# Optimization experiments

Measured on AMD Instinct MI355X. Metric: run time of the kernel, lower is better.

The kernel has to match this reference:

```python
import jax, jax.numpy as jnp
import numpy as np

N = 50000; E = 1600000; F_IN = 32; HEADS = 8; D = 16; HID = HEADS * D
ED = 16; G = 512; MH = 512; MO = 512; SLOPE = 0.2


def setup_inputs() -> dict:
    key = jax.random.key(0)
    ks = jax.random.split(key, 40)
    inp = {}
    inp["x"] = jax.random.normal(ks[0], (N, F_IN), jnp.float32)
    inp["edge_index"] = jax.random.randint(ks[1], (2, E), 0, N)
    inp["edge_attr"] = jax.random.normal(ks[2], (E, ED), jnp.float32)
    inp["batch"] = jnp.sort(jax.random.randint(ks[3], (N,), 0, G))

    def lin(k, fi, fo):
        return jax.random.normal(k, (fi, fo), jnp.float32) / np.sqrt(fi).astype(np.float32)

    i = 4
    dims = [(F_IN, HID), (HID, HID), (HID, HID)]  # GATv2 layers 0..2
    for l, (fi, fo) in enumerate(dims):
        inp[f"Wl{l}"] = lin(ks[i], fi, fo); i += 1
        inp[f"bl{l}"] = jnp.zeros((fo,), jnp.float32)
        inp[f"Wr{l}"] = lin(ks[i], fi, fo); i += 1
        inp[f"br{l}"] = jnp.zeros((fo,), jnp.float32)
        inp[f"We{l}"] = lin(ks[i], ED, fo); i += 1
        inp[f"att{l}"] = jax.random.normal(ks[i], (HEADS, D), jnp.float32) / np.sqrt(D).astype(np.float32); i += 1
        inp[f"b{l}"] = jnp.zeros((fo,), jnp.float32)
    inp["mW1"] = lin(ks[i], HID, MH); i += 1
    inp["mb1"] = jnp.zeros((MH,), jnp.float32)
    inp["ln_g"] = jnp.ones((MH,), jnp.float32)
    inp["ln_b"] = jnp.zeros((MH,), jnp.float32)
    inp["mW2"] = lin(ks[i], MH, MO); i += 1
    inp["mb2"] = jnp.zeros((MO,), jnp.float32)
    return inp


def _gatv2(h, src, dst, ea, Wl, bl, Wr, br, We, att, b):
    # One GATv2Conv layer (eval mode, add_self_loops already applied).
    n = h.shape[0]
    xl = (h @ Wl + bl).reshape(n, HEADS, D)   # source transform
    xr = (h @ Wr + br).reshape(n, HEADS, D)   # target transform
    ee = (ea @ We).reshape(-1, HEADS, D)      # edge transform (no bias in PyG)
    m = xl[src] + xr[dst] + ee                # [E', H, D]
    m = jnp.where(m > 0, m, SLOPE * m)        # LeakyReLU(0.2)
    s = jnp.einsum('ehd,hd->eh', m, att)      # attention logits
    mx = jax.ops.segment_max(s, dst, num_segments=n)
    ex = jnp.exp(s - mx[dst])
    den = jax.ops.segment_sum(ex, dst, num_segments=n)
    alpha = ex / den[dst]                     # softmax over incoming edges
    out = jax.ops.segment_sum(alpha[:, :, None] * xl[src], dst, num_segments=n)
    return out.reshape(n, HEADS * D) + b


def _forward(x, edge_index, edge_attr, batch,
             Wl0, bl0, Wr0, br0, We0, att0, b0,
             Wl1, bl1, Wr1, br1, We1, att1, b1,
             Wl2, bl2, Wr2, br2, We2, att2, b2,
             mW1, mb1, ln_g, ln_b, mW2, mb2):
    src, dst = edge_index[0], edge_index[1]
    # add_self_loops with fill_value='mean': self-loop edge_attr = mean of incoming edge_attr
    cnt = jax.ops.segment_sum(jnp.ones((E,), jnp.float32), dst, num_segments=N)
    loop_attr = jax.ops.segment_sum(edge_attr, dst, num_segments=N) / jnp.clip(cnt, 1.0)[:, None]
    nodes = jnp.arange(N)
    src_f = jnp.concatenate([src, nodes])
    dst_f = jnp.concatenate([dst, nodes])
    ea = jnp.concatenate([edge_attr, loop_attr], axis=0)

    h = jax.nn.relu(_gatv2(x, src_f, dst_f, ea, Wl0, bl0, Wr0, br0, We0, att0, b0))
    h = jax.nn.relu(_gatv2(h, src_f, dst_f, ea, Wl1, bl1, Wr1, br1, We1, att1, b1))
    h = _gatv2(h, src_f, dst_f, ea, Wl2, bl2, Wr2, br2, We2, att2, b2)

    g = jax.ops.segment_sum(h, batch, num_segments=G)  # sum pooling per graph
    z = jax.nn.relu(g @ mW1 + mb1)
    mu = jnp.mean(z, axis=-1, keepdims=True)
    var = jnp.var(z, axis=-1, keepdims=True)
    z = (z - mu) / jnp.sqrt(var + 1e-5) * ln_g + ln_b
    return z @ mW2 + mb2


def reference(x, edge_index, edge_attr, batch,
              Wl0, bl0, Wr0, br0, We0, att0, b0,
              Wl1, bl1, Wr1, br1, We1, att1, b1,
              Wl2, bl2, Wr2, br2, We2, att2, b2,
              mW1, mb1, ln_g, ln_b, mW2, mb2):
    return _forward(x, edge_index, edge_attr, batch,
                    Wl0, bl0, Wr0, br0, We0, att0, b0,
                    Wl1, bl1, Wr1, br1, We1, att1, b1,
                    Wl2, bl2, Wr2, br2, We2, att2, b2,
                    mW1, mb1, ln_g, ln_b, mW2, mb2)
```

## Files before the change

kernel.cpp:

```cpp
#include <hip/hip_runtime.h>
#include <hip/hip_fp16.h>
#include <math.h>

#define NN 50000
#define EE 1600000
#define FIN 32
#define HID_ 128
#define ED_ 16
#define GG 512
#define MH_ 512
#define MO_ 512

typedef float v2f __attribute__((ext_vector_type(2)));

#if __has_builtin(__builtin_amdgcn_exp2f)
#define EXP2(x) __builtin_amdgcn_exp2f(x)
#else
#define EXP2(x) exp2f(x)
#endif

template <int CTRL>
__device__ __forceinline__ float dpp_add(float x) {
  int m = __builtin_amdgcn_update_dpp(0, __float_as_int(x), CTRL, 0xF, 0xF, true);
  return x + __int_as_float(m);
}

__device__ __forceinline__ float bfly8(float p) {
  p = dpp_add<0xB1>(p);
  p = dpp_add<0x4E>(p);
  p = dpp_add<0x141>(p);
  return p;
}

__device__ __forceinline__ v2f h2f(__half2 h) {
  float2 f = __half22float2(h);
  return (v2f){f.x, f.y};
}


__global__ void hist_kernel(const int4* __restrict__ dst4, int* __restrict__ cnt) {
  int e = blockIdx.x * 256 + threadIdx.x;
  if (e >= EE / 4) return;
  int4 d = dst4[e];
  atomicAdd(&cnt[d.x], 1);
  atomicAdd(&cnt[d.y], 1);
  atomicAdd(&cnt[d.z], 1);
  atomicAdd(&cnt[d.w], 1);
}

__global__ __launch_bounds__(256) void scan1_kernel(const int* __restrict__ in, int n,
                                                    int* __restrict__ out,
                                                    int* __restrict__ bsums) {
  int chunk = blockIdx.x;
  int base = chunk * 1024;
  int t = threadIdx.x;
  int idx = base + t * 4;
  int v0 = (idx + 0 < n) ? in[idx + 0] : 0;
  int v1 = (idx + 1 < n) ? in[idx + 1] : 0;
  int v2 = (idx + 2 < n) ? in[idx + 2] : 0;
  int v3 = (idx + 3 < n) ? in[idx + 3] : 0;
  int ts = v0 + v1 + v2 + v3;
  int lane = t & 63, w = t >> 6;
  int s = ts;
#pragma unroll
  for (int off = 1; off < 64; off <<= 1) {
    int o = __shfl_up(s, off);
    if (lane >= off) s += o;
  }
  __shared__ int wsum[4];
  if (lane == 63) wsum[w] = s;
  __syncthreads();
  int woff = 0;
  for (int i = 0; i < w; i++) woff += wsum[i];
  int excl = woff + s - ts;
  int run = excl;
  run += v0; if (idx + 0 < n) out[idx + 0] = run;
  run += v1; if (idx + 1 < n) out[idx + 1] = run;
  run += v2; if (idx + 2 < n) out[idx + 2] = run;
  run += v3; if (idx + 3 < n) out[idx + 3] = run;
  if (t == 255) bsums[chunk] = woff + s;
}

__global__ void scan_add_kernel(int* __restrict__ rowptr, const int* __restrict__ bscan, int n) {
  int i = blockIdx.x * 256 + threadIdx.x;
  if (i == 0) rowptr[0] = 0;
  if (i < n) {
    int chunk = i >> 10;
    if (chunk > 0) rowptr[1 + i] += bscan[chunk - 1];
  }
}

__global__ void scatter_kernel(const int4* __restrict__ src4, const int4* __restrict__ dst4,
                               const int* __restrict__ rowptr, int* __restrict__ fill,
                               int2* __restrict__ csr) {
  int e = blockIdx.x * 256 + threadIdx.x;
  if (e >= EE / 4) return;
  int4 s = src4[e];
  int4 d = dst4[e];
  int eb = e * 4;
  int p0 = rowptr[d.x] + atomicAdd(&fill[d.x], 1);
  csr[p0] = make_int2(s.x, eb + 0);
  int p1 = rowptr[d.y] + atomicAdd(&fill[d.y], 1);
  csr[p1] = make_int2(s.y, eb + 1);
  int p2 = rowptr[d.z] + atomicAdd(&fill[d.z], 1);
  csr[p2] = make_int2(s.z, eb + 2);
  int p3 = rowptr[d.w] + atomicAdd(&fill[d.w], 1);
  csr[p3] = make_int2(s.w, eb + 3);
}


template <int F>
__global__ __launch_bounds__(256) void node_transform(const float* __restrict__ h,
                                                      const float* __restrict__ Wlm,
                                                      const float* __restrict__ blm,
                                                      const float* __restrict__ Wrm,
                                                      const float* __restrict__ brm,
                                                      __half2* __restrict__ xl,
                                                      __half2* __restrict__ xr, int nnodes) {
  __shared__ float hs[F * 34];
  int v0 = blockIdx.x * 32;
  int t = threadIdx.x;
  for (int idx = t; idx < 32 * F; idx += 256) {
    int i = idx / F, k = idx - i * F;
    hs[k * 34 + i] = (v0 + i < nnodes) ? h[(size_t)(v0 + i) * F + k] : 0.f;
  }
  __syncthreads();
  bool isL = t < 128;
  int q = t & 63;
  int nh = (t >> 6) & 1;
  const float* Wm = isL ? Wlm : Wrm;
  v2f acc[16];
#pragma unroll
  for (int i = 0; i < 16; i++) acc[i] = (v2f){0.f, 0.f};
  for (int k = 0; k < F; k++) {
    v2f w = *(const v2f*)(Wm + k * 128 + 2 * q);
    const v2f* hk2 = (const v2f*)(hs + k * 34 + nh * 16);
#pragma unroll
    for (int r = 0; r < 8; r++) {
      v2f hv = hk2[r];
      acc[2 * r + 0] = __builtin_elementwise_fma((v2f){hv.x, hv.x}, w, acc[2 * r + 0]);
      acc[2 * r + 1] = __builtin_elementwise_fma((v2f){hv.y, hv.y}, w, acc[2 * r + 1]);
    }
  }
  const float* bm = isL ? blm : brm;
  v2f b = *(const v2f*)(bm + 2 * q);
  __half2* dstp = isL ? xl : xr;
  int base = v0 + nh * 16;
#pragma unroll
  for (int i = 0; i < 16; i++) {
    if (base + i < nnodes) {
      v2f o = acc[i] + b;
      dstp[(size_t)(base + i) * 64 + q] = __floats2half2_rn(o.x, o.y);
    }
  }
}


template <int LAYER0>
__global__ __launch_bounds__(256) void gat_aggregate(
    const __half2* __restrict__ xl, const __half2* __restrict__ xr,
    const int* __restrict__ rowptr, const int2* __restrict__ csr,
    const float* __restrict__ ea, float* __restrict__ la,
    const float* __restrict__ We, const float* __restrict__ att,
    const float* __restrict__ bias, float* __restrict__ hout, int relu) {
  int wid = threadIdx.x >> 6, lane = threadIdx.x & 63;
  int v = __builtin_amdgcn_readfirstlane(blockIdx.x * 4 + wid);
  if (v >= NN) return;
  int c = 2 * lane;
  v2f wec[16];
#pragma unroll
  for (int k = 0; k < 16; k++) wec[k] = *(const v2f*)(We + k * 128 + c);
  const float L2E = 1.44269504088896340736f;
  v2f av = *(const v2f*)(att + c) * L2E;
  v2f xrv = h2f(xr[(size_t)v * 64 + lane]);

  auto score = [&](int u, const float* eaP, v2f& xu) -> float {
    xu = h2f(xl[(size_t)u * 64 + lane]);
    v2f m = xrv + xu;
#pragma unroll
    for (int k = 0; k < 16; k++) {
      float e = eaP[k];
      m = __builtin_elementwise_fma((v2f){e, e}, wec[k], m);
    }
    m = __builtin_elementwise_max(m, 0.2f * m);
    v2f qq = av * m;
    return bfly8(qq.x + qq.y);
  };

  int d16 = lane & 15;
  v2f acc = (v2f){0.f, 0.f};
  float den = 0.f;
  float la_f = 0.f;
  if (!LAYER0) {
    v2f xu;
    float p = score(v, la + (size_t)v * 16, xu);
    float w = EXP2(p);
    den = w;
    acc = (v2f){w, w} * xu;
  }
  int start = __builtin_amdgcn_readfirstlane(rowptr[v]);
  int end = __builtin_amdgcn_readfirstlane(rowptr[v + 1]);
  int j = start;
  for (; j + 4 <= end; j += 4) {
    int2 e0 = csr[j], e1 = csr[j + 1], e2 = csr[j + 2], e3 = csr[j + 3];
    int u0 = __builtin_amdgcn_readfirstlane(e0.x);
    int u1 = __builtin_amdgcn_readfirstlane(e1.x);
    int u2 = __builtin_amdgcn_readfirstlane(e2.x);
    int u3 = __builtin_amdgcn_readfirstlane(e3.x);
    const float* p0 = ea + (size_t)__builtin_amdgcn_readfirstlane(e0.y) * 16;
    const float* p1 = ea + (size_t)__builtin_amdgcn_readfirstlane(e1.y) * 16;
    const float* p2 = ea + (size_t)__builtin_amdgcn_readfirstlane(e2.y) * 16;
    const float* p3 = ea + (size_t)__builtin_amdgcn_readfirstlane(e3.y) * 16;
    if (LAYER0) la_f += (p0[d16] + p1[d16]) + (p2[d16] + p3[d16]);
    v2f x0, x1, x2, x3;
    float s0 = score(u0, p0, x0);
    float s1 = score(u1, p1, x1);
    float s2 = score(u2, p2, x2);
    float s3 = score(u3, p3, x3);
    float w0 = EXP2(s0), w1 = EXP2(s1), w2 = EXP2(s2), w3 = EXP2(s3);
    den += (w0 + w1) + (w2 + w3);
    acc = __builtin_elementwise_fma((v2f){w0, w0}, x0,
          __builtin_elementwise_fma((v2f){w1, w1}, x1,
          __builtin_elementwise_fma((v2f){w2, w2}, x2,
          __builtin_elementwise_fma((v2f){w3, w3}, x3, acc))));
  }
  for (; j < end; ++j) {
    int2 e0 = csr[j];
    int u = __builtin_amdgcn_readfirstlane(e0.x);
    const float* p0 = ea + (size_t)__builtin_amdgcn_readfirstlane(e0.y) * 16;
    if (LAYER0) la_f += p0[d16];
    v2f xu;
    float p = score(u, p0, xu);
    float w = EXP2(p);
    den += w;
    acc = __builtin_elementwise_fma((v2f){w, w}, xu, acc);
  }
  if (LAYER0) {
    int deg = end - start;
    float invdeg = (deg > 0) ? 1.f / (float)deg : 0.f;
    la_f *= invdeg;
    if (lane < 16) la[(size_t)v * 16 + d16] = la_f;
    v2f xu = h2f(xl[(size_t)v * 64 + lane]);
    v2f m = xrv + xu;
#pragma unroll
    for (int k = 0; k < 16; k++) {
      float e = __int_as_float(__builtin_amdgcn_readlane(__float_as_int(la_f), k));
      m = __builtin_elementwise_fma((v2f){e, e}, wec[k], m);
    }
    m = __builtin_elementwise_max(m, 0.2f * m);
    v2f qq = av * m;
    float p = bfly8(qq.x + qq.y);
    float w = EXP2(p);
    den += w;
    acc = __builtin_elementwise_fma((v2f){w, w}, xu, acc);
  }
  float invd = 1.f / den;
  v2f bv = *(const v2f*)(bias + c);
  v2f o = __builtin_elementwise_fma(acc, (v2f){invd, invd}, bv);
  if (relu) o = __builtin_elementwise_max(o, (v2f){0.f, 0.f});
  *(v2f*)(hout + (size_t)v * 128 + c) = o;
}


__global__ void gptr_kernel(const int* __restrict__ batch, int* __restrict__ gptr) {
  int g = blockIdx.x * 256 + threadIdx.x;
  if (g > GG) return;
  int lo = 0, hi = NN;
  while (lo < hi) {
    int mid = (lo + hi) >> 1;
    if (batch[mid] < g) lo = mid + 1; else hi = mid;
  }
  gptr[g] = lo;
}

__global__ void pool_kernel(const float* __restrict__ h, const int* __restrict__ gptr,
                            float* __restrict__ gp) {
  int gi = blockIdx.x;
  int c = threadIdx.x;
  int s = gptr[gi], e = gptr[gi + 1];
  float acc = 0.f;
  for (int v = s; v < e; v++) acc += h[(size_t)v * 128 + c];
  gp[gi * 128 + c] = acc;
}

__global__ __launch_bounds__(256) void mlp1_kernel(const float* __restrict__ gp,
                                                   const float* __restrict__ mW1,
                                                   const float* __restrict__ mb1,
                                                   const float* __restrict__ lng,
                                                   const float* __restrict__ lnb,
                                                   float* __restrict__ z) {
  int row = blockIdx.x;
  int t = threadIdx.x;
  __shared__ float gs[128];
  if (t < 128) gs[t] = gp[row * 128 + t];
  __syncthreads();
  int c0 = t, c1 = t + 256;
  float z0 = 0.f, z1 = 0.f;
  for (int k = 0; k < 128; k++) {
    float gk = gs[k];
    z0 = fmaf(gk, mW1[k * 512 + c0], z0);
    z1 = fmaf(gk, mW1[k * 512 + c1], z1);
  }
  z0 += mb1[c0]; z1 += mb1[c1];
  z0 = fmaxf(z0, 0.f); z1 = fmaxf(z1, 0.f);
  float s = z0 + z1, q = z0 * z0 + z1 * z1;
#pragma unroll
  for (int off = 32; off > 0; off >>= 1) {
    s += __shfl_xor(s, off);
    q += __shfl_xor(q, off);
  }
  __shared__ float red[8];
  int lane = t & 63, w = t >> 6;
  if (lane == 0) { red[w] = s; red[4 + w] = q; }
  __syncthreads();
  float S = red[0] + red[1] + red[2] + red[3];
  float Q = red[4] + red[5] + red[6] + red[7];
  float mu = S / 512.f;
  float var = Q / 512.f - mu * mu;
  float inv = 1.f / sqrtf(var + 1e-5f);
  z[row * 512 + c0] = (z0 - mu) * inv * lng[c0] + lnb[c0];
  z[row * 512 + c1] = (z1 - mu) * inv * lng[c1] + lnb[c1];
}

__global__ __launch_bounds__(256) void mlp2_kernel(const float* __restrict__ z,
                                                   const float* __restrict__ mW2,
                                                   const float* __restrict__ mb2,
                                                   float* __restrict__ out) {
  int row = blockIdx.x;
  int t = threadIdx.x;
  __shared__ float zs[512];
  for (int i = t; i < 512; i += 256) zs[i] = z[row * 512 + i];
  __syncthreads();
  int c0 = t, c1 = t + 256;
  float o0 = 0.f, o1 = 0.f;
  for (int k = 0; k < 512; k++) {
    float zk = zs[k];
    o0 = fmaf(zk, mW2[k * 512 + c0], o0);
    o1 = fmaf(zk, mW2[k * 512 + c1], o1);
  }
  out[row * 512 + c0] = o0 + mb2[c0];
  out[row * 512 + c1] = o1 + mb2[c1];
}


extern "C" void kernel_launch(void* const* d_in, const int* in_sizes, int n_in,
                              void* d_out, int out_size, void* d_ws, size_t ws_size,
                              hipStream_t stream) {
  const float* x = (const float*)d_in[0];
  const int* ei = (const int*)d_in[1];
  const int* srcE = ei;
  const int* dstE = ei + EE;
  const float* ea = (const float*)d_in[2];
  const int* batch = (const int*)d_in[3];
  const float* Wl[3] = {(const float*)d_in[4], (const float*)d_in[11], (const float*)d_in[18]};
  const float* bl[3] = {(const float*)d_in[5], (const float*)d_in[12], (const float*)d_in[19]};
  const float* Wr[3] = {(const float*)d_in[6], (const float*)d_in[13], (const float*)d_in[20]};
  const float* br[3] = {(const float*)d_in[7], (const float*)d_in[14], (const float*)d_in[21]};
  const float* Wek[3] = {(const float*)d_in[8], (const float*)d_in[15], (const float*)d_in[22]};
  const float* attk[3] = {(const float*)d_in[9], (const float*)d_in[16], (const float*)d_in[23]};
  const float* bk[3] = {(const float*)d_in[10], (const float*)d_in[17], (const float*)d_in[24]};
  const float* mW1 = (const float*)d_in[25];
  const float* mb1 = (const float*)d_in[26];
  const float* lng = (const float*)d_in[27];
  const float* lnb = (const float*)d_in[28];
  const float* mW2 = (const float*)d_in[29];
  const float* mb2 = (const float*)d_in[30];
  float* outp = (float*)d_out;

  char* W = (char*)d_ws;
  size_t off = 0;
  auto take = [&](size_t b) -> void* {
    void* p = W + off;
    off += (b + 255) & ~(size_t)255;
    return p;
  };
  int* cnt = (int*)take(NN * 4);
  int* rowptr = (int*)take((NN + 1) * 4);
  int* bsums = (int*)take(64 * 4);
  int* bscan = (int*)take(64 * 4);
  int* dummy = (int*)take(64 * 4);
  int2* csr = (int2*)take((size_t)EE * 8);
  float* la = (float*)take((size_t)NN * 16 * 4);
  __half2* xl = (__half2*)take((size_t)NN * 64 * 4);
  __half2* xr = (__half2*)take((size_t)NN * 64 * 4);
  float* hbuf = (float*)take((size_t)NN * HID_ * 4);
  int* gptr = (int*)take((GG + 1) * 4);
  float* gpool = (float*)take((size_t)GG * HID_ * 4);
  float* z = (float*)take((size_t)GG * MH_ * 4);
  (void)ws_size; (void)n_in; (void)in_sizes; (void)out_size;

  hipMemsetAsync(cnt, 0, NN * 4, stream);
  hist_kernel<<<(EE / 4 + 255) / 256, 256, 0, stream>>>((const int4*)dstE, cnt);
  scan1_kernel<<<49, 256, 0, stream>>>(cnt, NN, rowptr + 1, bsums);
  scan1_kernel<<<1, 256, 0, stream>>>(bsums, 49, bscan, dummy);
  scan_add_kernel<<<(NN + 255) / 256, 256, 0, stream>>>(rowptr, bscan, NN);
  hipMemsetAsync(cnt, 0, NN * 4, stream);
  scatter_kernel<<<(EE / 4 + 255) / 256, 256, 0, stream>>>((const int4*)srcE, (const int4*)dstE,
                                                           rowptr, cnt, csr);

  for (int l = 0; l < 3; l++) {
    if (l == 0)
      node_transform<FIN><<<(NN + 31) / 32, 256, 0, stream>>>(x, Wl[0], bl[0], Wr[0], br[0],
                                                              xl, xr, NN);
    else
      node_transform<HID_><<<(NN + 31) / 32, 256, 0, stream>>>(hbuf, Wl[l], bl[l], Wr[l], br[l],
                                                               xl, xr, NN);
    if (l == 0)
      gat_aggregate<1><<<(NN + 3) / 4, 256, 0, stream>>>(xl, xr, rowptr, csr, ea, la,
                                                         Wek[0], attk[0], bk[0], hbuf, 1);
    else
      gat_aggregate<0><<<(NN + 3) / 4, 256, 0, stream>>>(xl, xr, rowptr, csr, ea, la,
                                                         Wek[l], attk[l], bk[l], hbuf,
                                                         (l < 2) ? 1 : 0);
  }

  gptr_kernel<<<3, 256, 0, stream>>>(batch, gptr);
  pool_kernel<<<GG, 128, 0, stream>>>(hbuf, gptr, gpool);
  mlp1_kernel<<<GG, 256, 0, stream>>>(gpool, mW1, mb1, lng, lnb, z);
  mlp2_kernel<<<GG, 256, 0, stream>>>(z, mW2, mb2, outp);
}
```

Before: 882.1 us.

## Split each node's incoming edges across four wavefronts with LDS reduction

The aggregation kernel now gives each destination node a full 256-thread block instead of one wavefront. The node's incoming edge list is split into four contiguous quarters, one per wavefront. Partial softmax denominators, weighted accumulators and layer-0 edge-attr sums are combined through shared memory, and wave 0 finishes the self-loop term and writes the output. This raises parallelism per node and cuts per-wave serial latency, but it costs four times as many waves, an extra barrier, and idle waves for low-degree nodes (average degree about 32).

```diff
diff --git a/kernel.cpp b/kernel.cpp
--- a/kernel.cpp
+++ b/kernel.cpp
@@ -163,10 +163,11 @@
     const float* __restrict__ ea, float* __restrict__ la,
     const float* __restrict__ We, const float* __restrict__ att,
     const float* __restrict__ bias, float* __restrict__ hout, int relu) {
-  int wid = threadIdx.x >> 6, lane = threadIdx.x & 63;
-  int v = __builtin_amdgcn_readfirstlane(blockIdx.x * 4 + wid);
-  if (v >= NN) return;
+  int v = blockIdx.x;
+  int wv = threadIdx.x >> 6;
+  int lane = threadIdx.x & 63;
   int c = 2 * lane;
+  int d16 = lane & 15;
   v2f wec[16];
 #pragma unroll
   for (int k = 0; k < 16; k++) wec[k] = *(const v2f*)(We + k * 128 + c);
@@ -187,21 +188,16 @@
     return bfly8(qq.x + qq.y);
   };
 
-  int d16 = lane & 15;
+  int start = rowptr[v], end = rowptr[v + 1];
+  int deg = end - start;
+  int q0 = start + ((deg * wv) >> 2);
+  int q1 = start + ((deg * (wv + 1)) >> 2);
+
   v2f acc = (v2f){0.f, 0.f};
   float den = 0.f;
   float la_f = 0.f;
-  if (!LAYER0) {
-    v2f xu;
-    float p = score(v, la + (size_t)v * 16, xu);
-    float w = EXP2(p);
-    den = w;
-    acc = (v2f){w, w} * xu;
-  }
-  int start = __builtin_amdgcn_readfirstlane(rowptr[v]);
-  int end = __builtin_amdgcn_readfirstlane(rowptr[v + 1]);
-  int j = start;
-  for (; j + 4 <= end; j += 4) {
+  int j = q0;
+  for (; j + 4 <= q1; j += 4) {
     int2 e0 = csr[j], e1 = csr[j + 1], e2 = csr[j + 2], e3 = csr[j + 3];
     int u0 = __builtin_amdgcn_readfirstlane(e0.x);
     int u1 = __builtin_amdgcn_readfirstlane(e1.x);
@@ -224,7 +220,7 @@
           __builtin_elementwise_fma((v2f){w2, w2}, x2,
           __builtin_elementwise_fma((v2f){w3, w3}, x3, acc))));
   }
-  for (; j < end; ++j) {
+  for (; j < q1; ++j) {
     int2 e0 = csr[j];
     int u = __builtin_amdgcn_readfirstlane(e0.x);
     const float* p0 = ea + (size_t)__builtin_amdgcn_readfirstlane(e0.y) * 16;
@@ -235,8 +231,23 @@
     den += w;
     acc = __builtin_elementwise_fma((v2f){w, w}, xu, acc);
   }
+
+  __shared__ float sden[4][64];
+  __shared__ float saccx[4][64];
+  __shared__ float saccy[4][64];
+  __shared__ float sla[4][64];
+  sden[wv][lane] = den;
+  saccx[wv][lane] = acc.x;
+  saccy[wv][lane] = acc.y;
+  if (LAYER0) sla[wv][lane] = la_f;
+  __syncthreads();
+  if (wv != 0) return;
+  den = (sden[0][lane] + sden[1][lane]) + (sden[2][lane] + sden[3][lane]);
+  acc.x = (saccx[0][lane] + saccx[1][lane]) + (saccx[2][lane] + saccx[3][lane]);
+  acc.y = (saccy[0][lane] + saccy[1][lane]) + (saccy[2][lane] + saccy[3][lane]);
+
   if (LAYER0) {
-    int deg = end - start;
+    la_f = (sla[0][lane] + sla[1][lane]) + (sla[2][lane] + sla[3][lane]);
     float invdeg = (deg > 0) ? 1.f / (float)deg : 0.f;
     la_f *= invdeg;
     if (lane < 16) la[(size_t)v * 16 + d16] = la_f;
@@ -250,6 +261,12 @@
     m = __builtin_elementwise_max(m, 0.2f * m);
     v2f qq = av * m;
     float p = bfly8(qq.x + qq.y);
+    float w = EXP2(p);
+    den += w;
+    acc = __builtin_elementwise_fma((v2f){w, w}, xu, acc);
+  } else {
+    v2f xu;
+    float p = score(v, la + (size_t)v * 16, xu);
     float w = EXP2(p);
     den += w;
     acc = __builtin_elementwise_fma((v2f){w, w}, xu, acc);
@@ -406,12 +423,12 @@
       node_transform<HID_><<<(NN + 31) / 32, 256, 0, stream>>>(hbuf, Wl[l], bl[l], Wr[l], br[l],
                                                                xl, xr, NN);
     if (l == 0)
-      gat_aggregate<1><<<(NN + 3) / 4, 256, 0, stream>>>(xl, xr, rowptr, csr, ea, la,
-                                                         Wek[0], attk[0], bk[0], hbuf, 1);
+      gat_aggregate<1><<<NN, 256, 0, stream>>>(xl, xr, rowptr, csr, ea, la,
+                                               Wek[0], attk[0], bk[0], hbuf, 1);
     else
-      gat_aggregate<0><<<(NN + 3) / 4, 256, 0, stream>>>(xl, xr, rowptr, csr, ea, la,
-                                                         Wek[l], attk[l], bk[l], hbuf,
-                                                         (l < 2) ? 1 : 0);
+      gat_aggregate<0><<<NN, 256, 0, stream>>>(xl, xr, rowptr, csr, ea, la,
+                                               Wek[l], attk[l], bk[l], hbuf,
+                                               (l < 2) ? 1 : 0);
   }
 
   gptr_kernel<<<3, 256, 0, stream>>>(batch, gptr);
```

After: 1.064 ms. 20.6% more time.

## Split edge attention scoring into separate edge-ordered kernel before CSR aggregation

Applied to the files above, without the earlier changes.

Adds an edge_score kernel that walks edges in original order, reading edge_attr contiguously, and computes per-head exp-scores into a new E×8 buffer. The aggregation kernels then only gather the precomputed weights and xl rows instead of doing random-access edge_attr reads and the 16-step edge projection per edge. The aim is to replace scattered 64-byte edge_attr gathers in CSR order with streaming reads. The cost is an extra 51 MB write and a scattered read of that buffer per layer, plus an additional launch and xr gathers by dst.

```diff
diff --git a/kernel.cpp b/kernel.cpp
--- a/kernel.cpp
+++ b/kernel.cpp
@@ -10,6 +10,7 @@
 #define GG 512
 #define MH_ 512
 #define MO_ 512
+#define ES_BLOCKS 4096
 
 typedef float v2f __attribute__((ext_vector_type(2)));
 
@@ -156,48 +157,77 @@
 }
 
 
-template <int LAYER0>
-__global__ __launch_bounds__(256) void gat_aggregate(
+__global__ __launch_bounds__(256) void edge_score(
+    const __half2* __restrict__ xl, const __half2* __restrict__ xr,
+    const int* __restrict__ srcE, const int* __restrict__ dstE,
+    const float* __restrict__ ea, const float* __restrict__ We,
+    const float* __restrict__ att, float* __restrict__ w) {
+  int lane = threadIdx.x & 63;
+  int gw = __builtin_amdgcn_readfirstlane(blockIdx.x * 4 + (threadIdx.x >> 6));
+  int c = 2 * lane;
+  v2f wec[16];
+#pragma unroll
+  for (int k = 0; k < 16; k++) wec[k] = *(const v2f*)(We + k * 128 + c);
+  const float L2E = 1.44269504088896340736f;
+  v2f av = *(const v2f*)(att + c) * L2E;
+  bool st = (lane & 7) == 0;
+  int hh = lane >> 3;
+  const int STRIDE = ES_BLOCKS * 4 * 4;
+
+  for (int e0 = gw * 4; e0 < EE; e0 += STRIDE) {
+    int u0 = srcE[e0 + 0], u1 = srcE[e0 + 1], u2 = srcE[e0 + 2], u3 = srcE[e0 + 3];
+    int d0 = dstE[e0 + 0], d1 = dstE[e0 + 1], d2 = dstE[e0 + 2], d3 = dstE[e0 + 3];
+    const float* p0 = ea + (size_t)(e0 + 0) * 16;
+    const float* p1 = ea + (size_t)(e0 + 1) * 16;
+    const float* p2 = ea + (size_t)(e0 + 2) * 16;
+    const float* p3 = ea + (size_t)(e0 + 3) * 16;
+    v2f m0 = h2f(xl[(size_t)u0 * 64 + lane]) + h2f(xr[(size_t)d0 * 64 + lane]);
+    v2f m1 = h2f(xl[(size_t)u1 * 64 + lane]) + h2f(xr[(size_t)d1 * 64 + lane]);
+    v2f m2 = h2f(xl[(size_t)u2 * 64 + lane]) + h2f(xr[(size_t)d2 * 64 + lane]);
+    v2f m3 = h2f(xl[(size_t)u3 * 64 + lane]) + h2f(xr[(size_t)d3 * 64 + lane]);
+#pragma unroll
+    for (int k = 0; k < 16; k++) {
+      v2f wk = wec[k];
+      m0 = __builtin_elementwise_fma((v2f){p0[k], p0[k]}, wk, m0);
+      m1 = __builtin_elementwise_fma((v2f){p1[k], p1[k]}, wk, m1);
+      m2 = __builtin_elementwise_fma((v2f){p2[k], p2[k]}, wk, m2);
+      m3 = __builtin_elementwise_fma((v2f){p3[k], p3[k]}, wk, m3);
+    }
+    m0 = __builtin_elementwise_max(m0, 0.2f * m0);
+    m1 = __builtin_elementwise_max(m1, 0.2f * m1);
+    m2 = __builtin_elementwise_max(m2, 0.2f * m2);
+    m3 = __builtin_elementwise_max(m3, 0.2f * m3);
+    v2f q0 = av * m0, q1 = av * m1, q2 = av * m2, q3 = av * m3;
+    float w0 = EXP2(bfly8(q0.x + q0.y));
+    float w1 = EXP2(bfly8(q1.x + q1.y));
+    float w2 = EXP2(bfly8(q2.x + q2.y));
+    float w3 = EXP2(bfly8(q3.x + q3.y));
+    if (st) {
+      w[(size_t)(e0 + 0) * 8 + hh] = w0;
+      w[(size_t)(e0 + 1) * 8 + hh] = w1;
+      w[(size_t)(e0 + 2) * 8 + hh] = w2;
+      w[(size_t)(e0 + 3) * 8 + hh] = w3;
+    }
+  }
+}
+
+
+__global__ __launch_bounds__(256) void gat_l0(
     const __half2* __restrict__ xl, const __half2* __restrict__ xr,
     const int* __restrict__ rowptr, const int2* __restrict__ csr,
-    const float* __restrict__ ea, float* __restrict__ la,
-    const float* __restrict__ We, const float* __restrict__ att,
-    const float* __restrict__ bias, float* __restrict__ hout, int relu) {
+    const float* __restrict__ ea, const float* __restrict__ wbuf,
+    float* __restrict__ la, const float* __restrict__ We,
+    const float* __restrict__ att, const float* __restrict__ bias,
+    float* __restrict__ hout) {
   int wid = threadIdx.x >> 6, lane = threadIdx.x & 63;
   int v = __builtin_amdgcn_readfirstlane(blockIdx.x * 4 + wid);
   if (v >= NN) return;
   int c = 2 * lane;
-  v2f wec[16];
-#pragma unroll
-  for (int k = 0; k < 16; k++) wec[k] = *(const v2f*)(We + k * 128 + c);
-  const float L2E = 1.44269504088896340736f;
-  v2f av = *(const v2f*)(att + c) * L2E;
-  v2f xrv = h2f(xr[(size_t)v * 64 + lane]);
-
-  auto score = [&](int u, const float* eaP, v2f& xu) -> float {
-    xu = h2f(xl[(size_t)u * 64 + lane]);
-    v2f m = xrv + xu;
-#pragma unroll
-    for (int k = 0; k < 16; k++) {
-      float e = eaP[k];
-      m = __builtin_elementwise_fma((v2f){e, e}, wec[k], m);
-    }
-    m = __builtin_elementwise_max(m, 0.2f * m);
-    v2f qq = av * m;
-    return bfly8(qq.x + qq.y);
-  };
-
   int d16 = lane & 15;
+  int hh = lane >> 3;
   v2f acc = (v2f){0.f, 0.f};
   float den = 0.f;
   float la_f = 0.f;
-  if (!LAYER0) {
-    v2f xu;
-    float p = score(v, la + (size_t)v * 16, xu);
-    float w = EXP2(p);
-    den = w;
-    acc = (v2f){w, w} * xu;
-  }
   int start = __builtin_amdgcn_readfirstlane(rowptr[v]);
   int end = __builtin_amdgcn_readfirstlane(rowptr[v + 1]);
   int j = start;
@@ -207,17 +237,20 @@
     int u1 = __builtin_amdgcn_readfirstlane(e1.x);
     int u2 = __builtin_amdgcn_readfirstlane(e2.x);
     int u3 = __builtin_amdgcn_readfirstlane(e3.x);
-    const float* p0 = ea + (size_t)__builtin_amdgcn_readfirstlane(e0.y) * 16;
-    const float* p1 = ea + (size_t)__builtin_amdgcn_readfirstlane(e1.y) * 16;
-    const float* p2 = ea + (size_t)__builtin_amdgcn_readfirstlane(e2.y) * 16;
-    const float* p3 = ea + (size_t)__builtin_amdgcn_readfirstlane(e3.y) * 16;
-    if (LAYER0) la_f += (p0[d16] + p1[d16]) + (p2[d16] + p3[d16]);
-    v2f x0, x1, x2, x3;
-    float s0 = score(u0, p0, x0);
-    float s1 = score(u1, p1, x1);
-    float s2 = score(u2, p2, x2);
-    float s3 = score(u3, p3, x3);
-    float w0 = EXP2(s0), w1 = EXP2(s1), w2 = EXP2(s2), w3 = EXP2(s3);
+    size_t i0 = (size_t)__builtin_amdgcn_readfirstlane(e0.y);
+    size_t i1 = (size_t)__builtin_amdgcn_readfirstlane(e1.y);
+    size_t i2 = (size_t)__builtin_amdgcn_readfirstlane(e2.y);
+    size_t i3 = (size_t)__builtin_amdgcn_readfirstlane(e3.y);
+    la_f += (ea[i0 * 16 + d16] + ea[i1 * 16 + d16]) +
+            (ea[i2 * 16 + d16] + ea[i3 * 16 + d16]);
+    float w0 = wbuf[i0 * 8 + hh];
+    float w1 = wbuf[i1 * 8 + hh];
+    float w2 = wbuf[i2 * 8 + hh];
+    float w3 = wbuf[i3 * 8 + hh];
+    v2f x0 = h2f(xl[(size_t)u0 * 64 + lane]);
+    v2f x1 = h2f(xl[(size_t)u1 * 64 + lane]);
+    v2f x2 = h2f(xl[(size_t)u2 * 64 + lane]);
+    v2f x3 = h2f(xl[(size_t)u3 * 64 + lane]);
     den += (w0 + w1) + (w2 + w3);
     acc = __builtin_elementwise_fma((v2f){w0, w0}, x0,
           __builtin_elementwise_fma((v2f){w1, w1}, x1,
@@ -227,21 +260,25 @@
   for (; j < end; ++j) {
     int2 e0 = csr[j];
     int u = __builtin_amdgcn_readfirstlane(e0.x);
-    const float* p0 = ea + (size_t)__builtin_amdgcn_readfirstlane(e0.y) * 16;
-    if (LAYER0) la_f += p0[d16];
-    v2f xu;
-    float p = score(u, p0, xu);
-    float w = EXP2(p);
-    den += w;
-    acc = __builtin_elementwise_fma((v2f){w, w}, xu, acc);
-  }
-  if (LAYER0) {
-    int deg = end - start;
-    float invdeg = (deg > 0) ? 1.f / (float)deg : 0.f;
-    la_f *= invdeg;
-    if (lane < 16) la[(size_t)v * 16 + d16] = la_f;
+    size_t i0 = (size_t)__builtin_amdgcn_readfirstlane(e0.y);
+    la_f += ea[i0 * 16 + d16];
+    float w0 = wbuf[i0 * 8 + hh];
+    v2f xu = h2f(xl[(size_t)u * 64 + lane]);
+    den += w0;
+    acc = __builtin_elementwise_fma((v2f){w0, w0}, xu, acc);
+  }
+  int deg = end - start;
+  float invdeg = (deg > 0) ? 1.f / (float)deg : 0.f;
+  la_f *= invdeg;
+  if (lane < 16) la[(size_t)v * 16 + d16] = la_f;
+  {
+    v2f wec[16];
+#pragma unroll
+    for (int k = 0; k < 16; k++) wec[k] = *(const v2f*)(We + k * 128 + c);
+    const float L2E = 1.44269504088896340736f;
+    v2f av = *(const v2f*)(att + c) * L2E;
     v2f xu = h2f(xl[(size_t)v * 64 + lane]);
-    v2f m = xrv + xu;
+    v2f m = h2f(xr[(size_t)v * 64 + lane]) + xu;
 #pragma unroll
     for (int k = 0; k < 16; k++) {
       float e = __int_as_float(__builtin_amdgcn_readlane(__float_as_int(la_f), k));
@@ -253,6 +290,83 @@
     float w = EXP2(p);
     den += w;
     acc = __builtin_elementwise_fma((v2f){w, w}, xu, acc);
+  }
+  float invd = 1.f / den;
+  v2f bv = *(const v2f*)(bias + c);
+  v2f o = __builtin_elementwise_fma(acc, (v2f){invd, invd}, bv);
+  o = __builtin_elementwise_max(o, (v2f){0.f, 0.f});
+  *(v2f*)(hout + (size_t)v * 128 + c) = o;
+}
+
+__global__ __launch_bounds__(256) void gat_rest(
+    const __half2* __restrict__ xl, const __half2* __restrict__ xr,
+    const int* __restrict__ rowptr, const int2* __restrict__ csr,
+    const float* __restrict__ wbuf, const float* __restrict__ la,
+    const float* __restrict__ We, const float* __restrict__ att,
+    const float* __restrict__ bias, float* __restrict__ hout, int relu) {
+  int wid = threadIdx.x >> 6, lane = threadIdx.x & 63;
+  int v = __builtin_amdgcn_readfirstlane(blockIdx.x * 4 + wid);
+  if (v >= NN) return;
+  int c = 2 * lane;
+  int hh = lane >> 3;
+  v2f acc;
+  float den;
+  {
+    v2f wec[16];
+#pragma unroll
+    for (int k = 0; k < 16; k++) wec[k] = *(const v2f*)(We + k * 128 + c);
+    const float L2E = 1.44269504088896340736f;
+    v2f av = *(const v2f*)(att + c) * L2E;
+    const float* laP = la + (size_t)v * 16;
+    v2f xu = h2f(xl[(size_t)v * 64 + lane]);
+    v2f m = h2f(xr[(size_t)v * 64 + lane]) + xu;
+#pragma unroll
+    for (int k = 0; k < 16; k++) {
+      float e = laP[k];
+      m = __builtin_elementwise_fma((v2f){e, e}, wec[k], m);
+    }
+    m = __builtin_elementwise_max(m, 0.2f * m);
+    v2f qq = av * m;
+    float p = bfly8(qq.x + qq.y);
+    float w = EXP2(p);
+    den = w;
+    acc = (v2f){w, w} * xu;
+  }
+  int start = __builtin_amdgcn_readfirstlane(rowptr[v]);
+  int end = __builtin_amdgcn_readfirstlane(rowptr[v + 1]);
+  int j = start;
+  for (; j + 4 <= end; j += 4) {
+    int2 e0 = csr[j], e1 = csr[j + 1], e2 = csr[j + 2], e3 = csr[j + 3];
+    int u0 = __builtin_amdgcn_readfirstlane(e0.x);
+    int u1 = __builtin_amdgcn_readfirstlane(e1.x);
+    int u2 = __builtin_amdgcn_readfirstlane(e2.x);
+    int u3 = __builtin_amdgcn_readfirstlane(e3.x);
+    size_t i0 = (size_t)__builtin_amdgcn_readfirstlane(e0.y);
+    size_t i1 = (size_t)__builtin_amdgcn_readfirstlane(e1.y);
+    size_t i2 = (size_t)__builtin_amdgcn_readfirstlane(e2.y);
+    size_t i3 = (size_t)__builtin_amdgcn_readfirstlane(e3.y);
+    float w0 = wbuf[i0 * 8 + hh];
+    float w1 = wbuf[i1 * 8 + hh];
+    float w2 = wbuf[i2 * 8 + hh];
+    float w3 = wbuf[i3 * 8 + hh];
+    v2f x0 = h2f(xl[(size_t)u0 * 64 + lane]);
+    v2f x1 = h2f(xl[(size_t)u1 * 64 + lane]);
+    v2f x2 = h2f(xl[(size_t)u2 * 64 + lane]);
+    v2f x3 = h2f(xl[(size_t)u3 * 64 + lane]);
+    den += (w0 + w1) + (w2 + w3);
+    acc = __builtin_elementwise_fma((v2f){w0, w0}, x0,
+          __builtin_elementwise_fma((v2f){w1, w1}, x1,
+          __builtin_elementwise_fma((v2f){w2, w2}, x2,
+          __builtin_elementwise_fma((v2f){w3, w3}, x3, acc))));
+  }
+  for (; j < end; ++j) {
+    int2 e0 = csr[j];
+    int u = __builtin_amdgcn_readfirstlane(e0.x);
+    size_t i0 = (size_t)__builtin_amdgcn_readfirstlane(e0.y);
+    float w0 = wbuf[i0 * 8 + hh];
+    v2f xu = h2f(xl[(size_t)u * 64 + lane]);
+    den += w0;
+    acc = __builtin_elementwise_fma((v2f){w0, w0}, xu, acc);
   }
   float invd = 1.f / den;
   v2f bv = *(const v2f*)(bias + c);
@@ -384,6 +498,7 @@
   __half2* xl = (__half2*)take((size_t)NN * 64 * 4);
   __half2* xr = (__half2*)take((size_t)NN * 64 * 4);
   float* hbuf = (float*)take((size_t)NN * HID_ * 4);
+  float* wbuf = (float*)take((size_t)EE * 8 * 4);
   int* gptr = (int*)take((GG + 1) * 4);
   float* gpool = (float*)take((size_t)GG * HID_ * 4);
   float* z = (float*)take((size_t)GG * MH_ * 4);
@@ -405,13 +520,14 @@
     else
       node_transform<HID_><<<(NN + 31) / 32, 256, 0, stream>>>(hbuf, Wl[l], bl[l], Wr[l], br[l],
                                                                xl, xr, NN);
+    edge_score<<<ES_BLOCKS, 256, 0, stream>>>(xl, xr, srcE, dstE, ea, Wek[l], attk[l], wbuf);
     if (l == 0)
-      gat_aggregate<1><<<(NN + 3) / 4, 256, 0, stream>>>(xl, xr, rowptr, csr, ea, la,
-                                                         Wek[0], attk[0], bk[0], hbuf, 1);
+      gat_l0<<<(NN + 3) / 4, 256, 0, stream>>>(xl, xr, rowptr, csr, ea, wbuf, la,
+                                               Wek[0], attk[0], bk[0], hbuf);
     else
-      gat_aggregate<0><<<(NN + 3) / 4, 256, 0, stream>>>(xl, xr, rowptr, csr, ea, la,
-                                                         Wek[l], attk[l], bk[l], hbuf,
-                                                         (l < 2) ? 1 : 0);
+      gat_rest<<<(NN + 3) / 4, 256, 0, stream>>>(xl, xr, rowptr, csr, wbuf, la,
+                                                 Wek[l], attk[l], bk[l], hbuf,
+                                                 (l < 2) ? 1 : 0);
   }
 
   gptr_kernel<<<3, 256, 0, stream>>>(batch, gptr);
```

After: 1.202 ms. 1.36x slower.
